# Performance work log

Hardware: AMD Instinct MI355X
Metric: run time of the kernel (lower is better)

Reference implementation:

```python
import jax, jax.numpy as jnp
import numpy as np

B, V = 128, 512
REZ = [56, 28, 14, 7]
CH = [64, 128, 256, 512]
C = sum(CH)  # 960


def _gauss_stack(x0, y0, sig, n_pix, size=1.0):
    # mass-normalized 2D gaussian pRF per voxel, grid over aperture `size`
    g = (np.arange(n_pix, dtype=np.float32) + 0.5) / n_pix * size - size / 2
    xx, yy = np.meshgrid(g, g)
    d2 = (xx[None] - x0[:, None, None]) ** 2 + (yy[None] - y0[:, None, None]) ** 2
    z = np.exp(-d2 / (2.0 * sig[:, None, None] ** 2))
    z = z / (z.sum(axis=(1, 2), keepdims=True) + 1e-8)
    return z.astype(np.float32)


def setup_inputs() -> dict:
    key = jax.random.key(0)
    ks = jax.random.split(key, 8)
    rng = np.random.default_rng(0)
    # per-voxel pRF models: (x, y, sigma)
    x0 = rng.uniform(-0.4, 0.4, V).astype(np.float32)
    y0 = rng.uniform(-0.4, 0.4, V).astype(np.float32)
    sig = rng.uniform(0.05, 0.3, V).astype(np.float32)
    inp = {}
    for k, (n, c) in enumerate(zip(REZ, CH)):
        inp[f'fmap{k}'] = jax.random.normal(ks[k], (B, c, n, n), dtype=jnp.float32)
        inp[f'prf{k}'] = jnp.asarray(_gauss_stack(x0, y0, sig, n))
    inp['weights'] = jax.random.normal(ks[4], (V, C), dtype=jnp.float32) * 0.1
    inp['bias'] = jax.random.normal(ks[5], (V,), dtype=jnp.float32)
    inp['features_m'] = jax.random.normal(ks[6], (C, V), dtype=jnp.float32)  # features_mt.T
    inp['features_s'] = jax.random.uniform(ks[7], (C, V), dtype=jnp.float32) + 0.5  # features_st.T, positive
    return inp


def reference(fmap0, fmap1, fmap2, fmap3, prf0, prf1, prf2, prf3,
              weights, bias, features_m, features_s):
    fmaps = (fmap0, fmap1, fmap2, fmap3)
    prfs = (prf0, prf1, prf2, prf3)
    # per-voxel gaussian spatial pooling at each resolution: [B,Ck,V]
    feats = jnp.concatenate(
        [jnp.einsum('bchw,vhw->bcv', fm, pr) for fm, pr in zip(fmaps, prfs)], axis=1)
    # normalize per (channel, voxel); _nonlinearity is None
    feats = (feats - features_m[None]) / features_s[None]
    # per-voxel linear readout: equivalent to transpose -> bmm -> squeeze -> t
    r = jnp.einsum('bcv,vc->bv', feats, weights) + bias[None]
    return r
```

## Files before the change

kernel.cpp:

```cpp
#include <hip/hip_runtime.h>


typedef float f32x4 __attribute__((ext_vector_type(4)));
typedef f32x4 __attribute__((aligned(4))) f32x4u;
typedef __bf16 bf16x4 __attribute__((ext_vector_type(4)));
typedef __bf16 bf16x8 __attribute__((ext_vector_type(8)));

#define TILE_E 8192
#define V_DIM 512
#define C_TOT 960
#define B_DIM 128

#define NBT 268
#define NRA 896
#define PREP_WP 1920
#define PREP_OFF 512
#define PREP_BLKS (NBT + NRA + PREP_WP + PREP_OFF)

#define GEMM_BLKS 6144

#define WP_BYTES 1966080L
#define BT_BYTES ((long)NBT * TILE_E * 2)
#define RA_BYTES ((long)NRA * TILE_E * 2)
#define WS_NEED  (WP_BYTES + BT_BYTES + RA_BYTES)

static __device__ __forceinline__ int swz_idx(int row, int k) {
  return row * 64 + (((k >> 3) ^ (row & 7)) << 3) + (k & 7);
}

__global__ __launch_bounds__(256, 3)
void gemm_all(const float* __restrict__ f0, const float* __restrict__ f1,
              const float* __restrict__ f2,
              const __bf16* __restrict__ bt,
              const __bf16* __restrict__ ra,
              const float* __restrict__ wp,
              float* __restrict__ out)
{
  __shared__ float  lds_af[TILE_E];
  __shared__ __bf16 lds_b[TILE_E];

  const int tid  = threadIdx.x;
  const int lane = tid & 63;
  const int wid  = tid >> 6;
  const int wm   = wid >> 1;
  const int wn   = wid & 1;

  const int bid   = blockIdx.x;
  const int sslot = bid >> 3;
  const int xcd   = bid & 7;
  const int w     = (((sslot >> 2) << 3) + xcd) * 4 + (sslot & 3);

  f32x4 acc[4][4];
#pragma unroll
  for (int i = 0; i < 4; ++i)
#pragma unroll
    for (int j = 0; j < 4; ++j)
      acc[i][j] = f32x4{0.f, 0.f, 0.f, 0.f};

  int Ck, Coff, bn_g, bn;
  long bm;

  if (w < 2560) {
    const float* fmap; int K, nst, bbase, y, s0k, sendk;
    if (w < 1024) {
      fmap = f0; K = 3136; nst = 49; bbase = 0; Ck = 64; Coff = 0;
      bn_g = w & 3; y = (w >> 2) & 63;
      const int z = w >> 8; s0k = z * 12; sendk = (z == 3) ? 49 : s0k + 12;
    } else if (w < 1536) {
      const int l = w - 1024;
      fmap = f1; K = 784; nst = 13; bbase = 196; Ck = 128; Coff = 64;
      bn_g = l & 3; y = l >> 2; s0k = 0; sendk = 12;
    } else {
      const int l = w - 1536;
      fmap = f2; K = 196; nst = 4; bbase = 248; Ck = 256; Coff = 192;
      bn_g = l & 3; y = l >> 2; s0k = 0; sendk = 3;
    }
    bm = (long)y * 128; bn = bn_g * 128;

    for (int ks = s0k; ks < sendk; ++ks) {
      __syncthreads();

      const float* ab = fmap + bm * (long)K + (long)ks * 64;
#pragma unroll
      for (int i = 0; i < 8; ++i) {
        const int seg = wid * 8 + i;
        const int cc  = seg * 64 + lane;
        const int row = cc >> 4;
        const int q4  = (cc & 15) ^ (row & 7);
        __builtin_amdgcn_global_load_lds(
            (const __attribute__((address_space(1))) void*)(ab + (long)row * K + q4 * 4),
            (__attribute__((address_space(3))) void*)(&lds_af[seg * 256]),
            16, 0, 0);
      }
      const __bf16* bsrc = bt + (long)(bbase + bn_g * nst + ks) * TILE_E;
#pragma unroll
      for (int i = 0; i < 4; ++i) {
        const int seg = wid * 4 + i;
        __builtin_amdgcn_global_load_lds(
            (const __attribute__((address_space(1))) void*)(bsrc + seg * 512 + lane * 8),
            (__attribute__((address_space(3))) void*)(&lds_b[seg * 512]),
            16, 0, 0);
      }
      __syncthreads();

#pragma unroll
      for (int kc = 0; kc < 2; ++kc) {
        const int q4a = kc * 8 + ((lane >> 4) << 1);
        const int cx  = kc * 4 + (lane >> 4);
        bf16x8 af[4], bfr[4];
#pragma unroll
        for (int i = 0; i < 4; ++i) {
          const int r = wm * 64 + i * 16 + (lane & 15);
          const f32x4 fa = *(const f32x4*)&lds_af[r * 64 + ((q4a ^ (r & 7)) << 2)];
          const f32x4 fb = *(const f32x4*)&lds_af[r * 64 + (((q4a + 1) ^ (r & 7)) << 2)];
          af[i] = bf16x8{(__bf16)fa[0], (__bf16)fa[1], (__bf16)fa[2], (__bf16)fa[3],
                         (__bf16)fb[0], (__bf16)fb[1], (__bf16)fb[2], (__bf16)fb[3]};
        }
#pragma unroll
        for (int j = 0; j < 4; ++j) {
          const int r = wn * 64 + j * 16 + (lane & 15);
          bfr[j] = *(const bf16x8*)&lds_b[r * 64 + ((cx ^ (r & 7)) << 3)];
        }
#pragma unroll
        for (int i = 0; i < 4; ++i)
#pragma unroll
          for (int j = 0; j < 4; ++j)
            acc[i][j] = __builtin_amdgcn_mfma_f32_16x16x32_bf16(af[i], bfr[j],
                                                                acc[i][j], 0, 0, 0);
      }
    }
  } else {
    const int l = w - 2560;
    int y, btile;
    long raidx;
    if (l < 512) {
      y = l >> 2; bn_g = l & 3; raidx = y;          Ck = 128; Coff = 64;
      btile = 196 + bn_g * 13 + 12;
    } else if (l < 1536) {
      const int m = l - 512;
      y = m >> 2; bn_g = m & 3; raidx = 128 + y;    Ck = 256; Coff = 192;
      btile = 248 + bn_g * 4 + 3;
    } else {
      const int m = l - 1536;
      y = m >> 2; bn_g = m & 3; raidx = 384 + y;    Ck = 512; Coff = 448;
      btile = 264 + bn_g;
    }
    bm = (long)y * 128; bn = bn_g * 128;

    __bf16* lds_ab = (__bf16*)lds_af;
    const __bf16* asrc = ra + raidx * TILE_E;
    const __bf16* bsrc = bt + (long)btile * TILE_E;
#pragma unroll
    for (int i = 0; i < 4; ++i) {
      const int seg = wid * 4 + i;
      __builtin_amdgcn_global_load_lds(
          (const __attribute__((address_space(1))) void*)(asrc + seg * 512 + lane * 8),
          (__attribute__((address_space(3))) void*)(&lds_ab[seg * 512]),
          16, 0, 0);
      __builtin_amdgcn_global_load_lds(
          (const __attribute__((address_space(1))) void*)(bsrc + seg * 512 + lane * 8),
          (__attribute__((address_space(3))) void*)(&lds_b[seg * 512]),
          16, 0, 0);
    }
    __syncthreads();

#pragma unroll
    for (int kc = 0; kc < 2; ++kc) {
      const int cx = kc * 4 + (lane >> 4);
      bf16x8 af[4], bfr[4];
#pragma unroll
      for (int i = 0; i < 4; ++i) {
        const int r = wm * 64 + i * 16 + (lane & 15);
        af[i] = *(const bf16x8*)&lds_ab[r * 64 + ((cx ^ (r & 7)) << 3)];
      }
#pragma unroll
      for (int j = 0; j < 4; ++j) {
        const int r = wn * 64 + j * 16 + (lane & 15);
        bfr[j] = *(const bf16x8*)&lds_b[r * 64 + ((cx ^ (r & 7)) << 3)];
      }
#pragma unroll
      for (int i = 0; i < 4; ++i)
#pragma unroll
        for (int j = 0; j < 4; ++j)
          acc[i][j] = __builtin_amdgcn_mfma_f32_16x16x32_bf16(af[i], bfr[j],
                                                              acc[i][j], 0, 0, 0);
    }
  }

  const long mbase = bm + wm * 64;
  const int  bidx  = (int)(mbase / Ck);
  const int  cbase = (int)(mbase % Ck) + Coff;
  const int  lrow  = ((lane >> 4) << 2);
  const int  lcol  = lane & 15;

#pragma unroll
  for (int j = 0; j < 4; ++j) {
    const int v = bn + wn * 64 + j * 16 + lcol;
    float s = 0.f;
#pragma unroll
    for (int i = 0; i < 4; ++i) {
      const int cg = cbase + i * 16 + lrow;
#pragma unroll
      for (int r = 0; r < 4; ++r)
        s += acc[i][j][r] * wp[(long)(cg + r) * V_DIM + v];
    }
    s += __shfl_xor(s, 16);
    s += __shfl_xor(s, 32);
    if (lane < 16)
      atomicAdd(&out[(long)bidx * V_DIM + v], s);
  }
}

static __device__ __forceinline__ void conv_tile(const float* __restrict__ src,
                                                 int K, long rbase, int ks,
                                                 __bf16* __restrict__ dst, int tid)
{
#pragma unroll
  for (int it = 0; it < 4; ++it) {
    const int u   = tid + it * 256;
    const int row = u >> 3;
    const int q8  = u & 7;
    const int k   = ((q8 ^ (row & 7)) << 3);
    const long gk = (long)ks * 64 + k;
    const float* sp = src + (rbase + row) * (long)K + gk;
    bf16x8 h;
    if (gk + 8 <= K) {
      const f32x4u a = *(const f32x4u*)sp;
      const f32x4u b = *(const f32x4u*)(sp + 4);
      h[0]=(__bf16)a[0]; h[1]=(__bf16)a[1]; h[2]=(__bf16)a[2]; h[3]=(__bf16)a[3];
      h[4]=(__bf16)b[0]; h[5]=(__bf16)b[1]; h[6]=(__bf16)b[2]; h[7]=(__bf16)b[3];
    } else {
#pragma unroll
      for (int e = 0; e < 8; ++e)
        h[e] = (__bf16)((gk + e < K) ? sp[e] : 0.f);
    }
    *(bf16x8*)&dst[(long)row * 64 + q8 * 8] = h;
  }
}

__global__ void prep_all(const float* __restrict__ f1, const float* __restrict__ f2,
                         const float* __restrict__ f3,
                         const float* __restrict__ p0, const float* __restrict__ p1,
                         const float* __restrict__ p2, const float* __restrict__ p3,
                         const float* __restrict__ weights,
                         const float* __restrict__ bias,
                         const float* __restrict__ fm,
                         const float* __restrict__ fs,
                         float* __restrict__ wp,
                         __bf16* __restrict__ bt,
                         __bf16* __restrict__ ra,
                         float* __restrict__ out)
{
  __shared__ float red[4];
  const int blk = blockIdx.x;
  const int tid = threadIdx.x;

  if (blk < NBT) {
    if (!bt) return;
    int t = blk; const float* src; int K, g, ks;
    if (t < 196)      { src = p0; K = 3136; g = t / 49; ks = t % 49; }
    else if (t < 248) { t -= 196; src = p1; K = 784; g = t / 13; ks = t % 13; }
    else if (t < 264) { t -= 248; src = p2; K = 196; g = t / 4;  ks = t % 4; }
    else              { t -= 264; src = p3; K = 49;  g = t;      ks = 0; }
    conv_tile(src, K, (long)g * 128, ks, bt + (long)blk * TILE_E, tid);
  } else if (blk < NBT + NRA) {
    if (!ra) return;
    const int t = blk - NBT; const float* src; int K, ks; long rbase;
    if (t < 128)      { src = f1; K = 784; ks = 12; rbase = (long)t * 128; }
    else if (t < 384) { src = f2; K = 196; ks = 3;  rbase = (long)(t - 128) * 128; }
    else              { src = f3; K = 49;  ks = 0;  rbase = (long)(t - 384) * 128; }
    conv_tile(src, K, rbase, ks, ra + (long)t * TILE_E, tid);
  } else if (blk < NBT + NRA + PREP_WP) {
    if (!wp) return;
    const int idx = (blk - NBT - NRA) * 256 + tid;
    const int c = idx >> 9;
    const int v = idx & (V_DIM - 1);
    wp[idx] = weights[(long)v * C_TOT + c] / fs[idx];
  } else {
    const int v = blk - (NBT + NRA + PREP_WP);
    float s = 0.f;
    for (int c = tid; c < C_TOT; c += 256) {
      const long i = (long)c * V_DIM + v;
      s += fm[i] * weights[(long)v * C_TOT + c] / fs[i];
    }
#pragma unroll
    for (int o = 32; o; o >>= 1) s += __shfl_down(s, o);
    if ((tid & 63) == 0) red[tid >> 6] = s;
    __syncthreads();
    if (tid < B_DIM) {
      const float off = bias[v] - (red[0] + red[1] + red[2] + red[3]);
      out[(long)tid * V_DIM + v] = off;
    }
  }
}

__global__ __launch_bounds__(256, 3)
void gemm_fb(const float* __restrict__ fmap, const float* __restrict__ prf,
             const float* __restrict__ weights, const float* __restrict__ fs,
             const float* __restrict__ wp, float* __restrict__ out,
             int Ck, int K, int Coff, int nsteps, int kchunks)
{
  __shared__ __bf16 lds_a[TILE_E];
  __shared__ __bf16 lds_b[TILE_E];
  const int tid = threadIdx.x, lane = tid & 63, wid = tid >> 6;
  const int wm = wid >> 1, wn = wid & 1;
  const long bm = (long)blockIdx.y * 128;
  const int bn = blockIdx.x * 128;
  const int z = blockIdx.z, qb = nsteps / kchunks, rb = nsteps % kchunks;
  const int s0 = z * qb + (z < rb ? z : rb);
  const int send = s0 + qb + (z < rb ? 1 : 0);

  f32x4 acc[4][4];
#pragma unroll
  for (int i = 0; i < 4; ++i)
#pragma unroll
    for (int j = 0; j < 4; ++j) acc[i][j] = f32x4{0.f, 0.f, 0.f, 0.f};

  for (int ks = s0; ks < send; ++ks) {
    __syncthreads();
#pragma unroll
    for (int i = 0; i < 8; ++i) {
      const int c = tid + i * 256, row = c >> 4, k0 = (c & 15) << 2;
      const long gk = (long)ks * 64 + k0;
      const float* ap = fmap + (bm + row) * (long)K + gk;
      const float* bp = prf + (long)(bn + row) * K + gk;
      float a[4], b[4];
#pragma unroll
      for (int e = 0; e < 4; ++e) {
        a[e] = (gk + e < K) ? ap[e] : 0.f;
        b[e] = (gk + e < K) ? bp[e] : 0.f;
      }
      bf16x4 ha = {(__bf16)a[0], (__bf16)a[1], (__bf16)a[2], (__bf16)a[3]};
      bf16x4 hb = {(__bf16)b[0], (__bf16)b[1], (__bf16)b[2], (__bf16)b[3]};
      *(bf16x4*)&lds_a[swz_idx(row, k0)] = ha;
      *(bf16x4*)&lds_b[swz_idx(row, k0)] = hb;
    }
    __syncthreads();
#pragma unroll
    for (int kc = 0; kc < 2; ++kc) {
      const int cx = kc * 4 + (lane >> 4);
      bf16x8 af[4], bfr[4];
#pragma unroll
      for (int i = 0; i < 4; ++i) {
        const int r = wm * 64 + i * 16 + (lane & 15);
        af[i] = *(const bf16x8*)&lds_a[r * 64 + ((cx ^ (r & 7)) << 3)];
      }
#pragma unroll
      for (int j = 0; j < 4; ++j) {
        const int r = wn * 64 + j * 16 + (lane & 15);
        bfr[j] = *(const bf16x8*)&lds_b[r * 64 + ((cx ^ (r & 7)) << 3)];
      }
#pragma unroll
      for (int i = 0; i < 4; ++i)
#pragma unroll
        for (int j = 0; j < 4; ++j)
          acc[i][j] = __builtin_amdgcn_mfma_f32_16x16x32_bf16(af[i], bfr[j],
                                                              acc[i][j], 0, 0, 0);
    }
  }

  const long mbase = bm + wm * 64;
  const int bidx = (int)(mbase / Ck);
  const int cbase = (int)(mbase % Ck) + Coff;
  const int lrow = ((lane >> 4) << 2), lcol = lane & 15;
#pragma unroll
  for (int j = 0; j < 4; ++j) {
    const int v = bn + wn * 64 + j * 16 + lcol;
    float s = 0.f;
#pragma unroll
    for (int i = 0; i < 4; ++i) {
      const int cg = cbase + i * 16 + lrow;
#pragma unroll
      for (int r = 0; r < 4; ++r) {
        const float wf = wp ? wp[(long)(cg + r) * V_DIM + v]
                            : weights[(long)v * C_TOT + cg + r]
                              / fs[(long)(cg + r) * V_DIM + v];
        s += acc[i][j][r] * wf;
      }
    }
    s += __shfl_xor(s, 16);
    s += __shfl_xor(s, 32);
    if (lane < 16) atomicAdd(&out[(long)bidx * V_DIM + v], s);
  }
}

extern "C" void kernel_launch(void* const* d_in, const int* in_sizes, int n_in,
                              void* d_out, int out_size, void* d_ws, size_t ws_size,
                              hipStream_t stream)
{
  const float* fmap0   = (const float*)d_in[0];
  const float* prf0    = (const float*)d_in[1];
  const float* fmap1   = (const float*)d_in[2];
  const float* prf1    = (const float*)d_in[3];
  const float* fmap2   = (const float*)d_in[4];
  const float* prf2    = (const float*)d_in[5];
  const float* fmap3   = (const float*)d_in[6];
  const float* prf3    = (const float*)d_in[7];
  const float* weights = (const float*)d_in[8];
  const float* bias    = (const float*)d_in[9];
  const float* fm      = (const float*)d_in[10];
  const float* fs      = (const float*)d_in[11];
  float* out = (float*)d_out;

  const bool has_wp = ws_size >= (size_t)WP_BYTES;
  const bool has_ws = ws_size >= (size_t)WS_NEED;
  float*  wp = has_wp ? (float*)d_ws : nullptr;
  __bf16* bt = has_ws ? (__bf16*)((char*)d_ws + WP_BYTES) : nullptr;
  __bf16* ra = has_ws ? (__bf16*)((char*)d_ws + WP_BYTES + BT_BYTES) : nullptr;

  prep_all<<<dim3(PREP_BLKS), dim3(256), 0, stream>>>(
      fmap1, fmap2, fmap3, prf0, prf1, prf2, prf3,
      weights, bias, fm, fs, wp, bt, ra, out);

  if (has_ws) {
    gemm_all<<<dim3(GEMM_BLKS), dim3(256), 0, stream>>>(
        fmap0, fmap1, fmap2, bt, ra, wp, out);
  } else {
    struct Scale { const float* fmap; const float* prf; int Ck, K, Coff, nst, kch; };
    const Scale sc[4] = {
      {fmap0, prf0,  64, 3136,   0, 49, 4},
      {fmap1, prf1, 128,  784,  64, 13, 2},
      {fmap2, prf2, 256,  196, 192,  4, 1},
      {fmap3, prf3, 512,   49, 448,  1, 1},
    };
    for (int k = 0; k < 4; ++k) {
      dim3 grid(4, B_DIM * sc[k].Ck / 128, sc[k].kch);
      gemm_fb<<<grid, dim3(256), 0, stream>>>(
          sc[k].fmap, sc[k].prf, weights, fs, wp, out,
          sc[k].Ck, sc[k].K, sc[k].Coff, sc[k].nst, sc[k].kch);
    }
  }
}
```

Measured before the change: 110.2 us.

## Double-buffer A tiles in LDS, load pRF B fragments directly to registers

Restructures the GEMM kernel to double-buffer the fp32 feature-map tile in LDS so the next K-step's global-to-LDS load overlaps the current MFMA work. The separate tail blocks for the last K-step are folded into the main blocks, which cuts the grid from 6144 to 4608 blocks. The pRF B tiles are now pre-packed in MFMA fragment order, so each wave loads them straight into registers without going through LDS. LDS doubles and occupancy drops to 2 blocks per CU, and the wave priority is raised around the MFMA sections.

```diff
diff --git a/kernel.cpp b/kernel.cpp
--- a/kernel.cpp
+++ b/kernel.cpp
@@ -17,27 +17,31 @@
 #define PREP_OFF 512
 #define PREP_BLKS (NBT + NRA + PREP_WP + PREP_OFF)
 
-#define GEMM_BLKS 6144
+#define GEMM_BLKS 4608
 
 #define WP_BYTES 1966080L
 #define BT_BYTES ((long)NBT * TILE_E * 2)
 #define RA_BYTES ((long)NRA * TILE_E * 2)
 #define WS_NEED  (WP_BYTES + BT_BYTES + RA_BYTES)
 
+static __device__ __forceinline__ bf16x8 cvt8(f32x4 lo, f32x4 hi) {
+  return bf16x8{(__bf16)lo[0], (__bf16)lo[1], (__bf16)lo[2], (__bf16)lo[3],
+                (__bf16)hi[0], (__bf16)hi[1], (__bf16)hi[2], (__bf16)hi[3]};
+}
+
 static __device__ __forceinline__ int swz_idx(int row, int k) {
   return row * 64 + (((k >> 3) ^ (row & 7)) << 3) + (k & 7);
 }
 
-__global__ __launch_bounds__(256, 3)
-void gemm_all(const float* __restrict__ f0, const float* __restrict__ f1,
-              const float* __restrict__ f2,
-              const __bf16* __restrict__ bt,
-              const __bf16* __restrict__ ra,
-              const float* __restrict__ wp,
-              float* __restrict__ out)
+__global__ __launch_bounds__(256, 2)
+void gemm_main(const float* __restrict__ f0, const float* __restrict__ f1,
+               const float* __restrict__ f2, const float* __restrict__ f3,
+               const __bf16* __restrict__ bt,
+               const __bf16* __restrict__ ra,
+               const float* __restrict__ wp,
+               float* __restrict__ out)
 {
-  __shared__ float  lds_af[TILE_E];
-  __shared__ __bf16 lds_b[TILE_E];
+  __shared__ float lds[2 * TILE_E];
 
   const int tid  = threadIdx.x;
   const int lane = tid & 63;
@@ -50,6 +54,31 @@
   const int xcd   = bid & 7;
   const int w     = (((sslot >> 2) << 3) + xcd) * 4 + (sslot & 3);
 
+  const float* fmap;
+  int K, nst, bbase, Ck, Coff, y, bn_g, s0k, nfull;
+  long raidx = -1;
+  if (w < 1024) {
+    fmap = f0; K = 3136; nst = 49; bbase = 0; Ck = 64; Coff = 0;
+    bn_g = w & 3; y = (w >> 2) & 63;
+    const int z = w >> 8;
+    s0k = z * 12; nfull = (z == 3) ? 13 : 12;
+  } else if (w < 1536) {
+    const int l = w - 1024;
+    fmap = f1; K = 784; nst = 13; bbase = 196; Ck = 128; Coff = 64;
+    bn_g = l & 3; y = l >> 2; s0k = 0; nfull = 12; raidx = y;
+  } else if (w < 2560) {
+    const int l = w - 1536;
+    fmap = f2; K = 196; nst = 4; bbase = 248; Ck = 256; Coff = 192;
+    bn_g = l & 3; y = l >> 2; s0k = 0; nfull = 3; raidx = 128 + y;
+  } else {
+    const int l = w - 2560;
+    fmap = f3; K = 49; nst = 1; bbase = 264; Ck = 512; Coff = 448;
+    bn_g = l & 3; y = l >> 2; s0k = 0; nfull = 0; raidx = 384 + y;
+  }
+  const long bm = (long)y * 128;
+  const int  bn = bn_g * 128;
+  const bool tail = (raidx >= 0);
+
   f32x4 acc[4][4];
 #pragma unroll
   for (int i = 0; i < 4; ++i)
@@ -57,134 +86,106 @@
     for (int j = 0; j < 4; ++j)
       acc[i][j] = f32x4{0.f, 0.f, 0.f, 0.f};
 
-  int Ck, Coff, bn_g, bn;
-  long bm;
-
-  if (w < 2560) {
-    const float* fmap; int K, nst, bbase, y, s0k, sendk;
-    if (w < 1024) {
-      fmap = f0; K = 3136; nst = 49; bbase = 0; Ck = 64; Coff = 0;
-      bn_g = w & 3; y = (w >> 2) & 63;
-      const int z = w >> 8; s0k = z * 12; sendk = (z == 3) ? 49 : s0k + 12;
-    } else if (w < 1536) {
-      const int l = w - 1024;
-      fmap = f1; K = 784; nst = 13; bbase = 196; Ck = 128; Coff = 64;
-      bn_g = l & 3; y = l >> 2; s0k = 0; sendk = 12;
-    } else {
-      const int l = w - 1536;
-      fmap = f2; K = 196; nst = 4; bbase = 248; Ck = 256; Coff = 192;
-      bn_g = l & 3; y = l >> 2; s0k = 0; sendk = 3;
-    }
-    bm = (long)y * 128; bn = bn_g * 128;
-
-    for (int ks = s0k; ks < sendk; ++ks) {
-      __syncthreads();
-
-      const float* ab = fmap + bm * (long)K + (long)ks * 64;
-#pragma unroll
-      for (int i = 0; i < 8; ++i) {
-        const int seg = wid * 8 + i;
-        const int cc  = seg * 64 + lane;
-        const int row = cc >> 4;
-        const int q4  = (cc & 15) ^ (row & 7);
-        __builtin_amdgcn_global_load_lds(
-            (const __attribute__((address_space(1))) void*)(ab + (long)row * K + q4 * 4),
-            (__attribute__((address_space(3))) void*)(&lds_af[seg * 256]),
-            16, 0, 0);
-      }
-      const __bf16* bsrc = bt + (long)(bbase + bn_g * nst + ks) * TILE_E;
-#pragma unroll
-      for (int i = 0; i < 4; ++i) {
-        const int seg = wid * 4 + i;
-        __builtin_amdgcn_global_load_lds(
-            (const __attribute__((address_space(1))) void*)(bsrc + seg * 512 + lane * 8),
-            (__attribute__((address_space(3))) void*)(&lds_b[seg * 512]),
-            16, 0, 0);
-      }
-      __syncthreads();
-
-#pragma unroll
-      for (int kc = 0; kc < 2; ++kc) {
-        const int q4a = kc * 8 + ((lane >> 4) << 1);
-        const int cx  = kc * 4 + (lane >> 4);
-        bf16x8 af[4], bfr[4];
-#pragma unroll
-        for (int i = 0; i < 4; ++i) {
-          const int r = wm * 64 + i * 16 + (lane & 15);
-          const f32x4 fa = *(const f32x4*)&lds_af[r * 64 + ((q4a ^ (r & 7)) << 2)];
-          const f32x4 fb = *(const f32x4*)&lds_af[r * 64 + (((q4a + 1) ^ (r & 7)) << 2)];
-          af[i] = bf16x8{(__bf16)fa[0], (__bf16)fa[1], (__bf16)fa[2], (__bf16)fa[3],
-                         (__bf16)fb[0], (__bf16)fb[1], (__bf16)fb[2], (__bf16)fb[3]};
-        }
-#pragma unroll
-        for (int j = 0; j < 4; ++j) {
-          const int r = wn * 64 + j * 16 + (lane & 15);
-          bfr[j] = *(const bf16x8*)&lds_b[r * 64 + ((cx ^ (r & 7)) << 3)];
-        }
-#pragma unroll
-        for (int i = 0; i < 4; ++i)
-#pragma unroll
-          for (int j = 0; j < 4; ++j)
-            acc[i][j] = __builtin_amdgcn_mfma_f32_16x16x32_bf16(af[i], bfr[j],
-                                                                acc[i][j], 0, 0, 0);
-      }
-    }
-  } else {
-    const int l = w - 2560;
-    int y, btile;
-    long raidx;
-    if (l < 512) {
-      y = l >> 2; bn_g = l & 3; raidx = y;          Ck = 128; Coff = 64;
-      btile = 196 + bn_g * 13 + 12;
-    } else if (l < 1536) {
-      const int m = l - 512;
-      y = m >> 2; bn_g = m & 3; raidx = 128 + y;    Ck = 256; Coff = 192;
-      btile = 248 + bn_g * 4 + 3;
-    } else {
-      const int m = l - 1536;
-      y = m >> 2; bn_g = m & 3; raidx = 384 + y;    Ck = 512; Coff = 448;
-      btile = 264 + bn_g;
-    }
-    bm = (long)y * 128; bn = bn_g * 128;
-
-    __bf16* lds_ab = (__bf16*)lds_af;
+  const __bf16* btbase = bt + (long)(bbase + bn_g * nst) * TILE_E;
+
+  auto stage_a32 = [&](int off, int ks) {
+    const float* ab = fmap + bm * (long)K + (long)ks * 64;
+#pragma unroll
+    for (int i = 0; i < 8; ++i) {
+      const int seg = wid * 8 + i;
+      const int cc  = seg * 64 + lane;
+      const int row = cc >> 4;
+      const int q4  = (cc & 15) ^ (row & 7);
+      __builtin_amdgcn_global_load_lds(
+          (const __attribute__((address_space(1))) void*)(ab + (long)row * K + q4 * 4),
+          (__attribute__((address_space(3))) void*)(&lds[off + seg * 256]),
+          16, 0, 0);
+    }
+  };
+  auto stage_a16 = [&](int off) {
     const __bf16* asrc = ra + raidx * TILE_E;
-    const __bf16* bsrc = bt + (long)btile * TILE_E;
+    __bf16* dst = (__bf16*)&lds[off];
 #pragma unroll
     for (int i = 0; i < 4; ++i) {
       const int seg = wid * 4 + i;
       __builtin_amdgcn_global_load_lds(
           (const __attribute__((address_space(1))) void*)(asrc + seg * 512 + lane * 8),
-          (__attribute__((address_space(3))) void*)(&lds_ab[seg * 512]),
+          (__attribute__((address_space(3))) void*)(&dst[seg * 512]),
           16, 0, 0);
-      __builtin_amdgcn_global_load_lds(
-          (const __attribute__((address_space(1))) void*)(bsrc + seg * 512 + lane * 8),
-          (__attribute__((address_space(3))) void*)(&lds_b[seg * 512]),
-          16, 0, 0);
-    }
+    }
+  };
+  auto load_b = [&](int ks, bf16x8* br) {
+    const __bf16* tbp = btbase + (long)ks * TILE_E;
+#pragma unroll
+    for (int j = 0; j < 4; ++j)
+#pragma unroll
+      for (int kc = 0; kc < 2; ++kc)
+        br[j * 2 + kc] = *(const bf16x8*)(
+            tbp + ((((wn * 4 + j) * 2 + kc) << 6) + lane) * 8);
+  };
+
+  if (nfull > 0) stage_a32(0, s0k);
+  else if (tail) stage_a16(0);
+  __syncthreads();
+
+  int p = 0;
+  for (int t = 0; t < nfull; ++t) {
+    const int ks = s0k + t;
+    const int ro = p * TILE_E;
+    const int wo = (p ^ 1) * TILE_E;
+
+    bf16x8 breg[8];
+    load_b(ks, breg);
+    if (t + 1 < nfull)      stage_a32(wo, ks + 1);
+    else if (tail)          stage_a16(wo);
+
+    __builtin_amdgcn_s_setprio(1);
+#pragma unroll
+    for (int kc = 0; kc < 2; ++kc) {
+      const int q4a = kc * 8 + ((lane >> 4) << 1);
+      bf16x8 af[4];
+#pragma unroll
+      for (int i = 0; i < 4; ++i) {
+        const int r = wm * 64 + i * 16 + (lane & 15);
+        const f32x4 fa = *(const f32x4*)&lds[ro + r * 64 + ((q4a ^ (r & 7)) << 2)];
+        const f32x4 fb = *(const f32x4*)&lds[ro + r * 64 + (((q4a + 1) ^ (r & 7)) << 2)];
+        af[i] = cvt8(fa, fb);
+      }
+#pragma unroll
+      for (int i = 0; i < 4; ++i)
+#pragma unroll
+        for (int j = 0; j < 4; ++j)
+          acc[i][j] = __builtin_amdgcn_mfma_f32_16x16x32_bf16(
+              af[i], breg[j * 2 + kc], acc[i][j], 0, 0, 0);
+    }
+    __builtin_amdgcn_s_setprio(0);
+
     __syncthreads();
-
+    p ^= 1;
+  }
+
+  if (tail) {
+    const __bf16* lb = (const __bf16*)&lds[p * TILE_E];
+    bf16x8 breg[8];
+    load_b(nfull, breg);
+    __builtin_amdgcn_s_setprio(1);
 #pragma unroll
     for (int kc = 0; kc < 2; ++kc) {
       const int cx = kc * 4 + (lane >> 4);
-      bf16x8 af[4], bfr[4];
+      bf16x8 af[4];
 #pragma unroll
       for (int i = 0; i < 4; ++i) {
         const int r = wm * 64 + i * 16 + (lane & 15);
-        af[i] = *(const bf16x8*)&lds_ab[r * 64 + ((cx ^ (r & 7)) << 3)];
-      }
-#pragma unroll
-      for (int j = 0; j < 4; ++j) {
-        const int r = wn * 64 + j * 16 + (lane & 15);
-        bfr[j] = *(const bf16x8*)&lds_b[r * 64 + ((cx ^ (r & 7)) << 3)];
+        af[i] = *(const bf16x8*)&lb[r * 64 + ((cx ^ (r & 7)) << 3)];
       }
 #pragma unroll
       for (int i = 0; i < 4; ++i)
 #pragma unroll
         for (int j = 0; j < 4; ++j)
-          acc[i][j] = __builtin_amdgcn_mfma_f32_16x16x32_bf16(af[i], bfr[j],
-                                                              acc[i][j], 0, 0, 0);
-    }
+          acc[i][j] = __builtin_amdgcn_mfma_f32_16x16x32_bf16(
+              af[i], breg[j * 2 + kc], acc[i][j], 0, 0, 0);
+    }
+    __builtin_amdgcn_s_setprio(0);
   }
 
   const long mbase = bm + wm * 64;
@@ -225,10 +226,7 @@
     const float* sp = src + (rbase + row) * (long)K + gk;
     bf16x8 h;
     if (gk + 8 <= K) {
-      const f32x4u a = *(const f32x4u*)sp;
-      const f32x4u b = *(const f32x4u*)(sp + 4);
-      h[0]=(__bf16)a[0]; h[1]=(__bf16)a[1]; h[2]=(__bf16)a[2]; h[3]=(__bf16)a[3];
-      h[4]=(__bf16)b[0]; h[5]=(__bf16)b[1]; h[6]=(__bf16)b[2]; h[7]=(__bf16)b[3];
+      h = cvt8(*(const f32x4u*)sp, *(const f32x4u*)(sp + 4));
     } else {
 #pragma unroll
       for (int e = 0; e < 8; ++e)
@@ -262,7 +260,26 @@
     else if (t < 248) { t -= 196; src = p1; K = 784; g = t / 13; ks = t % 13; }
     else if (t < 264) { t -= 248; src = p2; K = 196; g = t / 4;  ks = t % 4; }
     else              { t -= 264; src = p3; K = 49;  g = t;      ks = 0; }
-    conv_tile(src, K, (long)g * 128, ks, bt + (long)blk * TILE_E, tid);
+    __bf16* dst = bt + (long)blk * TILE_E;
+#pragma unroll
+    for (int it = 0; it < 4; ++it) {
+      const int c2 = tid + it * 256;
+      const int fj = c2 >> 7;
+      const int kc = (c2 >> 6) & 1;
+      const int l  = c2 & 63;
+      const int row  = g * 128 + fj * 16 + (l & 15);
+      const int kcol = ks * 64 + kc * 32 + ((l >> 4) << 3);
+      const float* sp = src + (long)row * K + kcol;
+      bf16x8 h;
+      if (kcol + 8 <= K) {
+        h = cvt8(*(const f32x4u*)sp, *(const f32x4u*)(sp + 4));
+      } else {
+#pragma unroll
+        for (int e = 0; e < 8; ++e)
+          h[e] = (__bf16)((kcol + e < K) ? sp[e] : 0.f);
+      }
+      *(bf16x8*)&dst[(long)c2 * 8] = h;
+    }
   } else if (blk < NBT + NRA) {
     if (!ra) return;
     const int t = blk - NBT; const float* src; int K, ks; long rbase;
@@ -413,8 +430,8 @@
       weights, bias, fm, fs, wp, bt, ra, out);
 
   if (has_ws) {
-    gemm_all<<<dim3(GEMM_BLKS), dim3(256), 0, stream>>>(
-        fmap0, fmap1, fmap2, bt, ra, wp, out);
+    gemm_main<<<dim3(GEMM_BLKS), dim3(256), 0, stream>>>(
+        fmap0, fmap1, fmap2, fmap3, bt, ra, wp, out);
   } else {
     struct Scale { const float* fmap; const float* prf; int Ck, K, Coff, nst, kch; };
     const Scale sc[4] = {
```

Measured after the change: 119.3 us. 8.3% more time.

## Prepack B tiles in MFMA fragment order, load to registers, transpose readout weights

Applied to the files above, without the earlier changes.

The pRF B tiles are now pre-packed in the prep kernel in MFMA fragment order, so gemm_all reads them straight into registers with vector loads and no longer stages them through LDS. This removes the B half of the shared memory, and launch bounds are raised to 4 blocks per CU. The scaled readout weights are stored transposed as [V][C], so the epilogue fetches four consecutive channels with one float4 load instead of four strided loads. The costs are more registers per thread under the higher occupancy target, and B fragments that are no longer shared through LDS between the two waves with the same wn.

```diff
diff --git a/kernel.cpp b/kernel.cpp
--- a/kernel.cpp
+++ b/kernel.cpp
@@ -24,20 +24,24 @@
 #define RA_BYTES ((long)NRA * TILE_E * 2)
 #define WS_NEED  (WP_BYTES + BT_BYTES + RA_BYTES)
 
+static __device__ __forceinline__ bf16x8 cvt8(f32x4 lo, f32x4 hi) {
+  return bf16x8{(__bf16)lo[0], (__bf16)lo[1], (__bf16)lo[2], (__bf16)lo[3],
+                (__bf16)hi[0], (__bf16)hi[1], (__bf16)hi[2], (__bf16)hi[3]};
+}
+
 static __device__ __forceinline__ int swz_idx(int row, int k) {
   return row * 64 + (((k >> 3) ^ (row & 7)) << 3) + (k & 7);
 }
 
-__global__ __launch_bounds__(256, 3)
+__global__ __launch_bounds__(256, 4)
 void gemm_all(const float* __restrict__ f0, const float* __restrict__ f1,
               const float* __restrict__ f2,
               const __bf16* __restrict__ bt,
               const __bf16* __restrict__ ra,
-              const float* __restrict__ wp,
+              const float* __restrict__ wpt,
               float* __restrict__ out)
 {
-  __shared__ float  lds_af[TILE_E];
-  __shared__ __bf16 lds_b[TILE_E];
+  __shared__ float lds_af[TILE_E];
 
   const int tid  = threadIdx.x;
   const int lane = tid & 63;
@@ -59,6 +63,15 @@
 
   int Ck, Coff, bn_g, bn;
   long bm;
+
+  auto load_b = [&](const __bf16* tbp, bf16x8* br) {
+#pragma unroll
+    for (int j = 0; j < 4; ++j)
+#pragma unroll
+      for (int kc = 0; kc < 2; ++kc)
+        br[j * 2 + kc] = *(const bf16x8*)(
+            tbp + ((((wn * 4 + j) * 2 + kc) << 6) + lane) * 8);
+  };
 
   if (w < 2560) {
     const float* fmap; int K, nst, bbase, y, s0k, sendk;
@@ -92,41 +105,28 @@
             (__attribute__((address_space(3))) void*)(&lds_af[seg * 256]),
             16, 0, 0);
       }
-      const __bf16* bsrc = bt + (long)(bbase + bn_g * nst + ks) * TILE_E;
-#pragma unroll
-      for (int i = 0; i < 4; ++i) {
-        const int seg = wid * 4 + i;
-        __builtin_amdgcn_global_load_lds(
-            (const __attribute__((address_space(1))) void*)(bsrc + seg * 512 + lane * 8),
-            (__attribute__((address_space(3))) void*)(&lds_b[seg * 512]),
-            16, 0, 0);
-      }
+      bf16x8 breg[8];
+      load_b(bt + (long)(bbase + bn_g * nst + ks) * TILE_E, breg);
+
       __syncthreads();
 
 #pragma unroll
       for (int kc = 0; kc < 2; ++kc) {
         const int q4a = kc * 8 + ((lane >> 4) << 1);
-        const int cx  = kc * 4 + (lane >> 4);
-        bf16x8 af[4], bfr[4];
+        bf16x8 af[4];
 #pragma unroll
         for (int i = 0; i < 4; ++i) {
           const int r = wm * 64 + i * 16 + (lane & 15);
           const f32x4 fa = *(const f32x4*)&lds_af[r * 64 + ((q4a ^ (r & 7)) << 2)];
           const f32x4 fb = *(const f32x4*)&lds_af[r * 64 + (((q4a + 1) ^ (r & 7)) << 2)];
-          af[i] = bf16x8{(__bf16)fa[0], (__bf16)fa[1], (__bf16)fa[2], (__bf16)fa[3],
-                         (__bf16)fb[0], (__bf16)fb[1], (__bf16)fb[2], (__bf16)fb[3]};
+          af[i] = cvt8(fa, fb);
         }
 #pragma unroll
-        for (int j = 0; j < 4; ++j) {
-          const int r = wn * 64 + j * 16 + (lane & 15);
-          bfr[j] = *(const bf16x8*)&lds_b[r * 64 + ((cx ^ (r & 7)) << 3)];
-        }
-#pragma unroll
         for (int i = 0; i < 4; ++i)
 #pragma unroll
           for (int j = 0; j < 4; ++j)
-            acc[i][j] = __builtin_amdgcn_mfma_f32_16x16x32_bf16(af[i], bfr[j],
-                                                                acc[i][j], 0, 0, 0);
+            acc[i][j] = __builtin_amdgcn_mfma_f32_16x16x32_bf16(
+                af[i], breg[j * 2 + kc], acc[i][j], 0, 0, 0);
       }
     }
   } else {
@@ -149,7 +149,6 @@
 
     __bf16* lds_ab = (__bf16*)lds_af;
     const __bf16* asrc = ra + raidx * TILE_E;
-    const __bf16* bsrc = bt + (long)btile * TILE_E;
 #pragma unroll
     for (int i = 0; i < 4; ++i) {
       const int seg = wid * 4 + i;
@@ -157,33 +156,26 @@
           (const __attribute__((address_space(1))) void*)(asrc + seg * 512 + lane * 8),
           (__attribute__((address_space(3))) void*)(&lds_ab[seg * 512]),
           16, 0, 0);
-      __builtin_amdgcn_global_load_lds(
-          (const __attribute__((address_space(1))) void*)(bsrc + seg * 512 + lane * 8),
-          (__attribute__((address_space(3))) void*)(&lds_b[seg * 512]),
-          16, 0, 0);
-    }
+    }
+    bf16x8 breg[8];
+    load_b(bt + (long)btile * TILE_E, breg);
     __syncthreads();
 
 #pragma unroll
     for (int kc = 0; kc < 2; ++kc) {
       const int cx = kc * 4 + (lane >> 4);
-      bf16x8 af[4], bfr[4];
+      bf16x8 af[4];
 #pragma unroll
       for (int i = 0; i < 4; ++i) {
         const int r = wm * 64 + i * 16 + (lane & 15);
         af[i] = *(const bf16x8*)&lds_ab[r * 64 + ((cx ^ (r & 7)) << 3)];
       }
 #pragma unroll
-      for (int j = 0; j < 4; ++j) {
-        const int r = wn * 64 + j * 16 + (lane & 15);
-        bfr[j] = *(const bf16x8*)&lds_b[r * 64 + ((cx ^ (r & 7)) << 3)];
-      }
-#pragma unroll
       for (int i = 0; i < 4; ++i)
 #pragma unroll
         for (int j = 0; j < 4; ++j)
-          acc[i][j] = __builtin_amdgcn_mfma_f32_16x16x32_bf16(af[i], bfr[j],
-                                                              acc[i][j], 0, 0, 0);
+          acc[i][j] = __builtin_amdgcn_mfma_f32_16x16x32_bf16(
+              af[i], breg[j * 2 + kc], acc[i][j], 0, 0, 0);
     }
   }
 
@@ -200,9 +192,9 @@
 #pragma unroll
     for (int i = 0; i < 4; ++i) {
       const int cg = cbase + i * 16 + lrow;
-#pragma unroll
-      for (int r = 0; r < 4; ++r)
-        s += acc[i][j][r] * wp[(long)(cg + r) * V_DIM + v];
+      const f32x4 w4 = *(const f32x4*)&wpt[(long)v * C_TOT + cg];
+      s += acc[i][j][0] * w4[0] + acc[i][j][1] * w4[1]
+         + acc[i][j][2] * w4[2] + acc[i][j][3] * w4[3];
     }
     s += __shfl_xor(s, 16);
     s += __shfl_xor(s, 32);
@@ -225,10 +217,7 @@
     const float* sp = src + (rbase + row) * (long)K + gk;
     bf16x8 h;
     if (gk + 8 <= K) {
-      const f32x4u a = *(const f32x4u*)sp;
-      const f32x4u b = *(const f32x4u*)(sp + 4);
-      h[0]=(__bf16)a[0]; h[1]=(__bf16)a[1]; h[2]=(__bf16)a[2]; h[3]=(__bf16)a[3];
-      h[4]=(__bf16)b[0]; h[5]=(__bf16)b[1]; h[6]=(__bf16)b[2]; h[7]=(__bf16)b[3];
+      h = cvt8(*(const f32x4u*)sp, *(const f32x4u*)(sp + 4));
     } else {
 #pragma unroll
       for (int e = 0; e < 8; ++e)
@@ -246,7 +235,7 @@
                          const float* __restrict__ bias,
                          const float* __restrict__ fm,
                          const float* __restrict__ fs,
-                         float* __restrict__ wp,
+                         float* __restrict__ wpt,
                          __bf16* __restrict__ bt,
                          __bf16* __restrict__ ra,
                          float* __restrict__ out)
@@ -262,7 +251,26 @@
     else if (t < 248) { t -= 196; src = p1; K = 784; g = t / 13; ks = t % 13; }
     else if (t < 264) { t -= 248; src = p2; K = 196; g = t / 4;  ks = t % 4; }
     else              { t -= 264; src = p3; K = 49;  g = t;      ks = 0; }
-    conv_tile(src, K, (long)g * 128, ks, bt + (long)blk * TILE_E, tid);
+    __bf16* dst = bt + (long)blk * TILE_E;
+#pragma unroll
+    for (int it = 0; it < 4; ++it) {
+      const int c2 = tid + it * 256;
+      const int fj = c2 >> 7;
+      const int kc = (c2 >> 6) & 1;
+      const int l  = c2 & 63;
+      const int row  = g * 128 + fj * 16 + (l & 15);
+      const int kcol = ks * 64 + kc * 32 + ((l >> 4) << 3);
+      const float* sp = src + (long)row * K + kcol;
+      bf16x8 h;
+      if (kcol + 8 <= K) {
+        h = cvt8(*(const f32x4u*)sp, *(const f32x4u*)(sp + 4));
+      } else {
+#pragma unroll
+        for (int e = 0; e < 8; ++e)
+          h[e] = (__bf16)((kcol + e < K) ? sp[e] : 0.f);
+      }
+      *(bf16x8*)&dst[(long)c2 * 8] = h;
+    }
   } else if (blk < NBT + NRA) {
     if (!ra) return;
     const int t = blk - NBT; const float* src; int K, ks; long rbase;
@@ -271,11 +279,11 @@
     else              { src = f3; K = 49;  ks = 0;  rbase = (long)(t - 384) * 128; }
     conv_tile(src, K, rbase, ks, ra + (long)t * TILE_E, tid);
   } else if (blk < NBT + NRA + PREP_WP) {
-    if (!wp) return;
+    if (!wpt) return;
     const int idx = (blk - NBT - NRA) * 256 + tid;
-    const int c = idx >> 9;
-    const int v = idx & (V_DIM - 1);
-    wp[idx] = weights[(long)v * C_TOT + c] / fs[idx];
+    const int v = idx / C_TOT;
+    const int c = idx - v * C_TOT;
+    wpt[idx] = weights[idx] / fs[(long)c * V_DIM + v];
   } else {
     const int v = blk - (NBT + NRA + PREP_WP);
     float s = 0.f;
@@ -297,7 +305,7 @@
 __global__ __launch_bounds__(256, 3)
 void gemm_fb(const float* __restrict__ fmap, const float* __restrict__ prf,
              const float* __restrict__ weights, const float* __restrict__ fs,
-             const float* __restrict__ wp, float* __restrict__ out,
+             float* __restrict__ out,
              int Ck, int K, int Coff, int nsteps, int kchunks)
 {
   __shared__ __bf16 lds_a[TILE_E];
@@ -372,9 +380,8 @@
       const int cg = cbase + i * 16 + lrow;
 #pragma unroll
       for (int r = 0; r < 4; ++r) {
-        const float wf = wp ? wp[(long)(cg + r) * V_DIM + v]
-                            : weights[(long)v * C_TOT + cg + r]
-                              / fs[(long)(cg + r) * V_DIM + v];
+        const float wf = weights[(long)v * C_TOT + cg + r]
+                         / fs[(long)(cg + r) * V_DIM + v];
         s += acc[i][j][r] * wf;
       }
     }
@@ -402,19 +409,18 @@
   const float* fs      = (const float*)d_in[11];
   float* out = (float*)d_out;
 
-  const bool has_wp = ws_size >= (size_t)WP_BYTES;
   const bool has_ws = ws_size >= (size_t)WS_NEED;
-  float*  wp = has_wp ? (float*)d_ws : nullptr;
-  __bf16* bt = has_ws ? (__bf16*)((char*)d_ws + WP_BYTES) : nullptr;
-  __bf16* ra = has_ws ? (__bf16*)((char*)d_ws + WP_BYTES + BT_BYTES) : nullptr;
+  float*  wpt = has_ws ? (float*)d_ws : nullptr;
+  __bf16* bt  = has_ws ? (__bf16*)((char*)d_ws + WP_BYTES) : nullptr;
+  __bf16* ra  = has_ws ? (__bf16*)((char*)d_ws + WP_BYTES + BT_BYTES) : nullptr;
 
   prep_all<<<dim3(PREP_BLKS), dim3(256), 0, stream>>>(
       fmap1, fmap2, fmap3, prf0, prf1, prf2, prf3,
-      weights, bias, fm, fs, wp, bt, ra, out);
+      weights, bias, fm, fs, wpt, bt, ra, out);
 
   if (has_ws) {
     gemm_all<<<dim3(GEMM_BLKS), dim3(256), 0, stream>>>(
-        fmap0, fmap1, fmap2, bt, ra, wp, out);
+        fmap0, fmap1, fmap2, bt, ra, wpt, out);
   } else {
     struct Scale { const float* fmap; const float* prf; int Ck, K, Coff, nst, kch; };
     const Scale sc[4] = {
@@ -426,7 +432,7 @@
     for (int k = 0; k < 4; ++k) {
       dim3 grid(4, B_DIM * sc[k].Ck / 128, sc[k].kch);
       gemm_fb<<<grid, dim3(256), 0, stream>>>(
-          sc[k].fmap, sc[k].prf, weights, fs, wp, out,
+          sc[k].fmap, sc[k].prf, weights, fs, out,
           sc[k].Ck, sc[k].K, sc[k].Coff, sc[k].nst, sc[k].kch);
     }
   }
```

Result: slower. 145.6 us (+32.1%).
